# Optimization experiments

Hardware: AMD Instinct MI355X
Metric: run time of the kernel (lower is better)

## Reference

```python
import jax, jax.numpy as jnp
import numpy as np

B, L = 128, 5000
D_MODEL, N_LAYERS, D_STATE, D_INNER, D_CONV, DT_RANK = 8, 4, 16, 16, 3, 1
HID, N_CLASSES = 64, 230


def setup_inputs():
    key = jax.random.key(0)
    ks = iter(jax.random.split(key, 32))
    nrm = lambda shape, s=0.02: jax.random.normal(next(ks), shape, jnp.float32) * s
    return {
        "x": jax.random.uniform(next(ks), (B, L), jnp.float32),
        "idx": jnp.arange(L, dtype=jnp.int32),
        "embed": nrm((L, D_MODEL), 1.0),
        "norm_w": jnp.ones((N_LAYERS, D_MODEL), jnp.float32),
        "in_proj_w": nrm((N_LAYERS, 2 * D_INNER, D_MODEL), 0.2),
        "conv_w": nrm((N_LAYERS, D_INNER, 1, D_CONV), 0.3),
        "conv_b": nrm((N_LAYERS, D_INNER)),
        "x_proj_w": nrm((N_LAYERS, DT_RANK + 2 * D_STATE, D_INNER), 0.2),
        "dt_proj_w": nrm((N_LAYERS, D_INNER, DT_RANK), 0.5),
        "dt_proj_b": nrm((N_LAYERS, D_INNER), 0.1),
        "A_log": jnp.broadcast_to(jnp.log(jnp.arange(1., D_STATE + 1.)), (N_LAYERS, D_INNER, D_STATE)).astype(jnp.float32),
        "Dp": jnp.ones((N_LAYERS, D_INNER), jnp.float32),
        "out_proj_w": nrm((N_LAYERS, D_MODEL, D_INNER), 0.2),
        "c1_w": nrm((HID, D_MODEL, 3), 0.2), "c1_b": nrm((HID,)),
        "c2_w": nrm((HID, HID, 3), 0.1), "c2_b": nrm((HID,)),
        "c3_w": nrm((HID, HID, 3), 0.1), "c3_b": nrm((HID,)),
        "fc_w": nrm((N_CLASSES, HID), 0.1), "fc_b": jnp.zeros((N_CLASSES,), jnp.float32),
    }


def _conv1d(x, w, b, pad, groups=1):
    # x: [B, C, L], w: [O, I/groups, K]
    y = jax.lax.conv_general_dilated(x, w, (1,), [pad], dimension_numbers=("NCH", "OIH", "NCH"), feature_group_count=groups)
    return y + b[None, :, None]


def _rmsnorm(x, w, eps=1e-5):
    return x * jax.lax.rsqrt(jnp.mean(x * x, -1, keepdims=True) + eps) * w


def _selective_scan(u, delta, A, Bm, Cm, Dv):
    # u, delta: [B, L, ED]; A: [ED, N]; Bm, Cm: [B, L, N]
    dA = jnp.exp(delta[..., None] * A)                       # [B, L, ED, N]
    dBu = delta[..., None] * Bm[:, :, None, :] * u[..., None]  # [B, L, ED, N]

    def step(h, t):
        dA_t, dBu_t, c_t = t
        h = dA_t * h + dBu_t                                  # [B, ED, N]
        return h, jnp.einsum("ben,bn->be", h, c_t)

    h0 = jnp.zeros((dA.shape[0], dA.shape[2], dA.shape[3]), u.dtype)
    _, ys = jax.lax.scan(step, h0, (dA.swapaxes(0, 1), dBu.swapaxes(0, 1), Cm.swapaxes(0, 1)))
    return ys.swapaxes(0, 1) + Dv * u


def reference(x, idx, embed, norm_w, in_proj_w, conv_w, conv_b, x_proj_w, dt_proj_w, dt_proj_b, A_log, Dp, out_proj_w, c1_w, c1_b, c2_w, c2_b, c3_w, c3_b, fc_w, fc_b):
    # embedding(idx) broadcast over batch, gated by intensities x
    f = embed[idx][None, :, :] * x[:, :, None]                # [B, L, D_MODEL]
    for l in range(N_LAYERS):
        xn = _rmsnorm(f, norm_w[l])
        xz = xn @ in_proj_w[l].T                              # [B, L, 2*ED]
        xc, z = xz[..., :D_INNER], xz[..., D_INNER:]
        xc = _conv1d(xc.swapaxes(1, 2), conv_w[l], conv_b[l], (D_CONV - 1, 0), D_INNER).swapaxes(1, 2)
        xc = jax.nn.silu(xc)
        dbc = xc @ x_proj_w[l].T                              # [B, L, dt_rank+2N]
        delta = jax.nn.softplus(dbc[..., :DT_RANK] @ dt_proj_w[l].T + dt_proj_b[l])
        Bm = dbc[..., DT_RANK:DT_RANK + D_STATE]
        Cm = dbc[..., DT_RANK + D_STATE:]
        y = _selective_scan(xc, delta, -jnp.exp(A_log[l]), Bm, Cm, Dp[l])
        f = (y * jax.nn.silu(z)) @ out_proj_w[l].T + f        # residual
    feat = f.swapaxes(1, 2)                                   # [B, D_MODEL, L]
    h = jax.nn.relu(_conv1d(feat, c1_w, c1_b, (1, 1)))
    r = jax.nn.relu(_conv1d(h, c2_w, c2_b, (1, 1)))
    r = _conv1d(r, c3_w, c3_b, (1, 1))
    h = jax.nn.relu(h + r)                                    # residual conv block
    pooled = h.mean(-1)                                       # [B, HID]
    return pooled @ fc_w.T + fc_b                             # [B, N_CLASSES]
```

## Files before the change

kernel.cpp:

```cpp
#include <hip/hip_runtime.h>
#include <math.h>

#define B 128
#define L 5000
#define NL 4
#define NCH 50
#define LC 100
#define ST 50
#define HT 128

typedef __attribute__((ext_vector_type(8))) short bf16x8;
typedef __attribute__((ext_vector_type(4))) short short4v;
typedef __attribute__((ext_vector_type(4))) float f32x4;

__device__ __forceinline__ float sigmoidf_(float x){ return 1.f/(1.f+__expf(-x)); }
__device__ __forceinline__ float siluf_(float x){ return x*sigmoidf_(x); }
__device__ __forceinline__ float softplusf_(float x){ return fmaxf(x,0.f) + log1pf(__expf(-fabsf(x))); }
__device__ __forceinline__ short bfc_(float x){
  union { float f; unsigned u; } v; v.f = x;
  unsigned r = v.u + 0x7fffu + ((v.u >> 16) & 1u);
  return (short)(r >> 16);
}
__device__ __forceinline__ float b2f_(short s){
  union { unsigned u; float f; } v; v.u = ((unsigned)(unsigned short)s) << 16;
  return v.f;
}
#define SW(row, col) (((row)<<6) + ((col) ^ (((row)&7)<<3)))

__global__ void k_embed(const float* __restrict__ x, const int* __restrict__ idx,
                        const float* __restrict__ embed, float* __restrict__ f){
  int gid = blockIdx.x*256 + threadIdx.x;
  if (gid >= B*L) return;
  int t = gid % L;
  float xv = x[gid];
  const float* er = embed + (size_t)idx[t]*8;
  float4 e0 = *(const float4*)(er);
  float4 e1 = *(const float4*)(er+4);
  *(float4*)(f + (size_t)gid*8)   = make_float4(e0.x*xv, e0.y*xv, e0.z*xv, e0.w*xv);
  *(float4*)(f + (size_t)gid*8+4) = make_float4(e1.x*xv, e1.y*xv, e1.z*xv, e1.w*xv);
}

__global__ __launch_bounds__(256,4) void k_l1(const float* __restrict__ fin,
    const float* __restrict__ norm_w, const float* __restrict__ in_proj,
    const float* __restrict__ conv_w, const float* __restrict__ conv_b,
    const float* __restrict__ x_proj, const float* __restrict__ dt_w,
    const float* __restrict__ dt_b, const float* __restrict__ A_log,
    float* __restrict__ Sc, float* __restrict__ Pc){
  __shared__ float fsub[52][8], rn[52];
  __shared__ float uL[ST][17];
  __shared__ float2 duL[ST][16];
  __shared__ float BLs[ST][17];
  __shared__ float dbc0[ST];
  int tid = threadIdx.x, ch = blockIdx.x, b = blockIdx.y;
  int e = tid>>4, n = tid&15;
  int ct = tid&15;
  float ipnw_c[8], cwc[3];
  #pragma unroll
  for (int d=0;d<8;d++) ipnw_c[d] = in_proj[ct*8+d]*norm_w[d];
  #pragma unroll
  for (int k=0;k<3;k++) cwc[k] = conv_w[ct*3+k];
  float cbc = conv_b[ct];
  float xp0_c = x_proj[ct];
  float xpB_r[16];
  #pragma unroll
  for (int k=0;k<16;k++) xpB_r[k] = x_proj[(1+ct)*16+k];
  float dtw_e = dt_w[ct], dtb_e = dt_b[ct];
  float a = -__expf(A_log[e*16+n]);
  float h = 0.f, dsum = 0.f;
  int t00 = ch*LC;
  for (int sub=0; sub<LC/ST; sub++){
    int ts = t00 + sub*ST;
    __syncthreads();
    for (int i=tid;i<104;i+=256){ int r=i>>1, half=i&1; int t=ts-2+r;
      *(float4*)&fsub[r][half*4] = (t>=0) ? *(const float4*)&fin[((size_t)b*L+t)*8+half*4]
                                          : make_float4(0.f,0.f,0.f,0.f); }
    __syncthreads();
    if (tid < 52){ float ss=0.f;
      #pragma unroll
      for (int d=0;d<8;d++){ float v=fsub[tid][d]; ss += v*v; }
      rn[tid] = rsqrtf(ss*0.125f + 1e-5f); }
    __syncthreads();
    for (int i=tid;i<ST*16;i+=256){ int j=i>>4;
      float acc = cbc;
      #pragma unroll
      for (int kk=0;kk<3;kk++){
        int r = j + kk;
        float dot=0.f;
        #pragma unroll
        for (int d=0;d<8;d++) dot += ipnw_c[d]*fsub[r][d];
        acc += cwc[kk]*(dot*rn[r]);
      }
      float uv = siluf_(acc);
      uL[j][ct] = uv;
      float pp = xp0_c*uv;
      pp += __shfl_xor(pp, 1, 64);
      pp += __shfl_xor(pp, 2, 64);
      pp += __shfl_xor(pp, 4, 64);
      pp += __shfl_xor(pp, 8, 64);
      if (ct == 0) dbc0[j] = pp;
    }
    __syncthreads();
    for (int i=tid;i<ST*16;i+=256){ int j=i>>4;
      float accB=0.f;
      #pragma unroll
      for (int c=0;c<16;c++) accB += xpB_r[c]*uL[j][c];
      BLs[j][ct] = accB;
      float dd = softplusf_(dbc0[j]*dtw_e + dtb_e);
      duL[j][ct] = make_float2(dd, dd*uL[j][ct]);
    }
    __syncthreads();
    for (int j=0;j<ST;j++){
      float2 du = duL[j][e];
      float bb = BLs[j][n];
      h = __expf(du.x*a)*h + du.y*bb;
      dsum += du.x;
    }
  }
  size_t o = ((size_t)b*NCH + ch)*256 + tid;
  Sc[o] = h;
  Pc[o] = __expf(a*dsum);
}

__global__ __launch_bounds__(256,4) void k_l3(const float* __restrict__ fin, float* __restrict__ fout,
    const float* __restrict__ norm_w, const float* __restrict__ in_proj,
    const float* __restrict__ conv_w, const float* __restrict__ conv_b,
    const float* __restrict__ x_proj, const float* __restrict__ dt_w,
    const float* __restrict__ dt_b, const float* __restrict__ A_log,
    const float* __restrict__ Dp, const float* __restrict__ Sc,
    const float* __restrict__ Pc, const float* __restrict__ ow){
  __shared__ float fsub[52][8], rn[52];
  __shared__ float uL[ST*16], szL[ST*16], yL[ST*16];
  __shared__ float2 duL[ST*16], BCL[ST*16];
  __shared__ float dbc0[ST];
  __shared__ float s_owp[8*17], s_De[16];
  __shared__ float hcL[10*320];
  int tid = threadIdx.x, ch = blockIdx.x, b = blockIdx.y;
  int e = tid>>4, n = tid&15;
  int ct = tid&15;
  int dt8 = tid&7;
  float ipnw_c[8], ipnwz_c[8], cwc[3];
  #pragma unroll
  for (int d=0;d<8;d++){
    ipnw_c[d]  = in_proj[ct*8+d]*norm_w[d];
    ipnwz_c[d] = in_proj[(16+ct)*8+d]*norm_w[d];
  }
  #pragma unroll
  for (int k=0;k<3;k++) cwc[k] = conv_w[ct*3+k];
  float cbc = conv_b[ct];
  float xp0_c = x_proj[ct];
  float xpB_r[16], xpC_r[16];
  #pragma unroll
  for (int k=0;k<16;k++){
    xpB_r[k] = x_proj[(1+ct)*16+k];
    xpC_r[k] = x_proj[(17+ct)*16+k];
  }
  float dtw_e = dt_w[ct], dtb_e = dt_b[ct];
  float a = -__expf(A_log[e*16+n]);
  if (tid < 128) s_owp[(tid>>4)*17 + (tid&15)] = ow[tid];
  if (tid < 16) s_De[tid] = Dp[tid];
  float h = 0.f;
  for (int c2=0; c2<ch; c2++){
    size_t o = ((size_t)b*NCH + c2)*256 + tid;
    h = Pc[o]*h + Sc[o];
  }
  int t00 = ch*LC;
  for (int sub=0; sub<LC/ST; sub++){
    int ts = t00 + sub*ST;
    __syncthreads();
    for (int i=tid;i<104;i+=256){ int r=i>>1, half=i&1; int t=ts-2+r;
      *(float4*)&fsub[r][half*4] = (t>=0) ? *(const float4*)&fin[((size_t)b*L+t)*8+half*4]
                                          : make_float4(0.f,0.f,0.f,0.f); }
    __syncthreads();
    if (tid < 52){ float ss=0.f;
      #pragma unroll
      for (int d=0;d<8;d++){ float v=fsub[tid][d]; ss += v*v; }
      rn[tid] = rsqrtf(ss*0.125f + 1e-5f); }
    __syncthreads();
    for (int i=tid;i<ST*16;i+=256){ int j=i>>4;
      float acc = cbc;
      #pragma unroll
      for (int kk=0;kk<3;kk++){
        int r = j + kk;
        float dot=0.f;
        #pragma unroll
        for (int d=0;d<8;d++) dot += ipnw_c[d]*fsub[r][d];
        acc += cwc[kk]*(dot*rn[r]);
      }
      float uv = siluf_(acc);
      uL[j*16+ct] = uv;
      int r2 = j + 2;
      float dz=0.f;
      #pragma unroll
      for (int d=0;d<8;d++) dz += ipnwz_c[d]*fsub[r2][d];
      szL[j*16+ct] = siluf_(dz*rn[r2]);
      float pp = xp0_c*uv;
      pp += __shfl_xor(pp, 1, 64);
      pp += __shfl_xor(pp, 2, 64);
      pp += __shfl_xor(pp, 4, 64);
      pp += __shfl_xor(pp, 8, 64);
      if (ct == 0) dbc0[j] = pp;
    }
    __syncthreads();
    for (int i=tid;i<ST*16;i+=256){ int j=i>>4;
      f32x4 u0 = *(const f32x4*)&uL[j*16];
      f32x4 u1 = *(const f32x4*)&uL[j*16+4];
      f32x4 u2 = *(const f32x4*)&uL[j*16+8];
      f32x4 u3 = *(const f32x4*)&uL[j*16+12];
      float accB=0.f, accC=0.f;
      #pragma unroll
      for (int c=0;c<4;c++){
        accB += xpB_r[c]*u0[c] + xpB_r[4+c]*u1[c] + xpB_r[8+c]*u2[c] + xpB_r[12+c]*u3[c];
        accC += xpC_r[c]*u0[c] + xpC_r[4+c]*u1[c] + xpC_r[8+c]*u2[c] + xpC_r[12+c]*u3[c];
      }
      BCL[j*16+ct] = make_float2(accB, accC);
      float dd = softplusf_(dbc0[j]*dtw_e + dtb_e);
      duL[j*16+ct] = make_float2(dd, dd*uL[j*16+ct]);
    }
    __syncthreads();
    for (int q=0; q<ST/10; q++){
      #pragma unroll
      for (int j2=0; j2<10; j2++){
        int j = q*10 + j2;
        float2 du = duL[j*16+e];
        float2 bc = BCL[j*16+n];
        h = __expf(du.x*a)*h + du.y*bc.x;
        hcL[j2*320 + e*20 + n] = h*bc.y;
      }
      __syncthreads();
      if (tid < 160){
        int jj = tid>>4, ee = tid&15;
        int j = q*10 + jj;
        const f32x4* hp = (const f32x4*)&hcL[jj*320 + ee*20];
        f32x4 p0 = hp[0], p1 = hp[1], p2 = hp[2], p3 = hp[3];
        float s = ((p0[0]+p0[1])+(p0[2]+p0[3])) + ((p1[0]+p1[1])+(p1[2]+p1[3]))
                + ((p2[0]+p2[1])+(p2[2]+p2[3])) + ((p3[0]+p3[1])+(p3[2]+p3[3]));
        yL[j*16+ee] = (s + s_De[ee]*uL[j*16+ee]) * szL[j*16+ee];
      }
      __syncthreads();
    }
    for (int i=tid;i<ST*8;i+=256){ int j=i>>3;
      size_t fi = ((size_t)b*L + ts + j)*8 + dt8;
      float acc = fsub[j+2][dt8];
      f32x4 y0 = *(const f32x4*)&yL[j*16];
      f32x4 y1 = *(const f32x4*)&yL[j*16+4];
      f32x4 y2 = *(const f32x4*)&yL[j*16+8];
      f32x4 y3 = *(const f32x4*)&yL[j*16+12];
      #pragma unroll
      for (int c=0;c<4;c++)
        acc += s_owp[dt8*17+c]*y0[c] + s_owp[dt8*17+4+c]*y1[c]
             + s_owp[dt8*17+8+c]*y2[c] + s_owp[dt8*17+12+c]*y3[c];
      fout[fi] = acc;
    }
  }
}

__global__ void k_wt(const float* __restrict__ c1w, const float* __restrict__ c2w,
                     const float* __restrict__ c3w, short* __restrict__ wt1b,
                     short* __restrict__ wt2b, short* __restrict__ wt3b){
  int idx = blockIdx.x*256 + threadIdx.x;
  if (idx < 2048){
    int c = idx >> 5, m = idx & 31;
    int kk = m >> 3, d = m & 7;
    wt1b[idx] = (kk < 3) ? bfc_(c1w[c*24 + d*3 + kk]) : (short)0;
  } else if (idx < 2048 + 12288){
    int i = idx - 2048;
    int c = i / 192, rem = i % 192;
    int k = rem >> 6, ci = rem & 63;
    wt2b[i] = bfc_(c2w[c*192 + ci*3 + k]);
  } else if (idx < 2048 + 24576){
    int i = idx - 2048 - 12288;
    int c = i / 192, rem = i % 192;
    int k = rem >> 6, ci = rem & 63;
    wt3b[i] = bfc_(c3w[c*192 + ci*3 + k]);
  }
}

__global__ __launch_bounds__(256) void k_head(const float* __restrict__ f,
   const short* __restrict__ wt1b, const float* __restrict__ c1b,
   const short* __restrict__ wt2b, const float* __restrict__ c2b,
   const short* __restrict__ wt3b, const float* __restrict__ c3b,
   float* __restrict__ pooled){
  __shared__ short fs_b[146*8];
  __shared__ short h1t[146*64];
  __shared__ short h2t[130*64];
  int tid  = threadIdx.x;
  int b    = blockIdx.y;
  int t0   = blockIdx.x * HT;
  int lane = tid & 63;
  int w    = tid >> 6;
  int cb   = w*16;
  int lc   = lane & 15, g = lane >> 4;

  for (int task = tid; task < 146*8; task += 256){
    int r = task >> 3, d = task & 7;
    int t = t0 - 3 + r;
    float v = (r < 134 && t >= 0 && t < L) ? f[((size_t)b*L + t)*8 + d] : 0.f;
    fs_b[task] = bfc_(v);
  }
  for (int i = tid; i < 14*64; i += 256){
    int row = 132 + (i>>6), col = i&63;
    h1t[SW(row, col)] = 0;
  }
  __syncthreads();

  {
    bf16x8 a1 = *(const bf16x8*)(wt1b + (cb + lc)*32 + g*8);
    f32x4 bias1 = *(const f32x4*)(c1b + cb + (g<<2));
    #pragma unroll
    for (int nt=0; nt<9; nt++){
      int tcol = nt*16 + lc;
      bf16x8 bv = {0,0,0,0,0,0,0,0};
      if (g < 3) bv = *(bf16x8*)&fs_b[(tcol+g)*8];
      f32x4 acc = {0.f,0.f,0.f,0.f};
      acc = __builtin_amdgcn_mfma_f32_16x16x32_bf16(a1, bv, acc, 0, 0, 0);
      if (tcol < 132){
        int t1 = t0 - 2 + tcol;
        bool v = (t1 >= 0 && t1 < L);
        short4v pk;
        #pragma unroll
        for (int reg=0;reg<4;reg++)
          pk[reg] = bfc_(v ? fmaxf(acc[reg] + bias1[reg], 0.f) : 0.f);
        *(short4v*)&h1t[SW(tcol, cb + (g<<2))] = pk;
      }
    }
  }
  __syncthreads();

  {
    const short* wA = wt2b + (cb + lc)*192 + g*8;
    bf16x8 a2[6];
    #pragma unroll
    for (int s=0;s<6;s++) a2[s] = *(const bf16x8*)(wA + 32*s);
    f32x4 bias2 = *(const f32x4*)(c2b + cb + (g<<2));
    #pragma unroll
    for (int nt=0; nt<9; nt++){
      f32x4 acc = {0.f,0.f,0.f,0.f};
      #pragma unroll
      for (int s=0;s<6;s++){
        int k = s>>1, ci0 = (s&1)*32;
        int jr = nt*16 + lc + k;
        bf16x8 bfr = *(bf16x8*)&h1t[SW(jr, ci0 + g*8)];
        acc = __builtin_amdgcn_mfma_f32_16x16x32_bf16(a2[s], bfr, acc, 0, 0, 0);
      }
      int tr = nt*16 + lc;
      if (tr < 130){
        int tg = t0 - 1 + tr;
        bool v = (tg >= 0 && tg < L);
        short4v pk;
        #pragma unroll
        for (int reg=0;reg<4;reg++)
          pk[reg] = bfc_(v ? fmaxf(acc[reg] + bias2[reg], 0.f) : 0.f);
        *(short4v*)&h2t[SW(tr, cb + (g<<2))] = pk;
      }
    }
  }
  __syncthreads();

  {
    const short* wA = wt3b + (cb + lc)*192 + g*8;
    bf16x8 a3[6];
    #pragma unroll
    for (int s=0;s<6;s++) a3[s] = *(const bf16x8*)(wA + 32*s);
    f32x4 bias3 = *(const f32x4*)(c3b + cb + (g<<2));
    int c0 = cb + (g<<2);
    float pool[4] = {0.f,0.f,0.f,0.f};
    #pragma unroll
    for (int nt=0; nt<8; nt++){
      f32x4 acc = {0.f,0.f,0.f,0.f};
      #pragma unroll
      for (int s=0;s<6;s++){
        int k = s>>1, ci0 = (s&1)*32;
        int jr = nt*16 + lc + k;
        bf16x8 bfr = *(bf16x8*)&h2t[SW(jr, ci0 + g*8)];
        acc = __builtin_amdgcn_mfma_f32_16x16x32_bf16(a3[s], bfr, acc, 0, 0, 0);
      }
      int t = t0 + nt*16 + lc;
      short4v hres = *(short4v*)&h1t[SW(nt*16 + lc + 2, c0)];
      if (t < L){
        #pragma unroll
        for (int reg=0;reg<4;reg++)
          pool[reg] += fmaxf(b2f_(hres[reg]) + acc[reg] + bias3[reg], 0.f);
      }
    }
    #pragma unroll
    for (int m=1; m<16; m<<=1){
      #pragma unroll
      for (int reg=0;reg<4;reg++) pool[reg] += __shfl_xor(pool[reg], m, 64);
    }
    if (lc == 0){
      #pragma unroll
      for (int reg=0;reg<4;reg++) atomicAdd(&pooled[b*64 + c0 + reg], pool[reg]);
    }
  }
}

__global__ void k_fc(const float* __restrict__ pooled, const float* __restrict__ fcw,
                     const float* __restrict__ fcb, float* __restrict__ out){
  int gid = blockIdx.x*256 + threadIdx.x;
  if (gid >= B*230) return;
  int b = gid / 230, j = gid % 230;
  const float* p = pooled + b*64;
  const float* wv = fcw + j*64;
  float a = 0.f;
  #pragma unroll
  for (int c=0;c<64;c++) a += p[c]*wv[c];
  out[gid] = a*(1.f/(float)L) + fcb[j];
}

extern "C" void kernel_launch(void* const* d_in, const int* in_sizes, int n_in,
                              void* d_out, int out_size, void* d_ws, size_t ws_size,
                              hipStream_t stream){
  const float* x      = (const float*)d_in[0];
  const int*   idx    = (const int*)  d_in[1];
  const float* embed  = (const float*)d_in[2];
  const float* norm_w = (const float*)d_in[3];
  const float* in_proj= (const float*)d_in[4];
  const float* conv_w = (const float*)d_in[5];
  const float* conv_b = (const float*)d_in[6];
  const float* x_proj = (const float*)d_in[7];
  const float* dt_w   = (const float*)d_in[8];
  const float* dt_b   = (const float*)d_in[9];
  const float* A_log  = (const float*)d_in[10];
  const float* Dp     = (const float*)d_in[11];
  const float* out_w  = (const float*)d_in[12];
  const float* c1w    = (const float*)d_in[13];
  const float* c1b    = (const float*)d_in[14];
  const float* c2w    = (const float*)d_in[15];
  const float* c2b    = (const float*)d_in[16];
  const float* c3w    = (const float*)d_in[17];
  const float* c3b    = (const float*)d_in[18];
  const float* fcw    = (const float*)d_in[19];
  const float* fcb    = (const float*)d_in[20];
  float* out = (float*)d_out;

  float* ws = (float*)d_ws;
  float* f0     = ws;
  float* f1     = f0 + 5120000;
  float* Sc     = f1 + 5120000;
  float* Pc     = Sc + 1638400;
  float* pooled = Pc + 1638400;
  short* wt1b   = (short*)(pooled + 8192);
  short* wt2b   = wt1b + 2048;
  short* wt3b   = wt2b + 12288;

  k_wt<<<104,256,0,stream>>>(c1w, c2w, c3w, wt1b, wt2b, wt3b);
  k_embed<<<2500,256,0,stream>>>(x, idx, embed, f0);
  for (int l=0;l<NL;l++){
    const float* fin = (l & 1) ? f1 : f0;
    float*       fo  = (l & 1) ? f0 : f1;
    k_l1<<<dim3(NCH,B),256,0,stream>>>(fin, norm_w + l*8, in_proj + l*256, conv_w + l*48,
         conv_b + l*16, x_proj + l*528, dt_w + l*16, dt_b + l*16, A_log + l*256, Sc, Pc);
    k_l3<<<dim3(NCH,B),256,0,stream>>>(fin, fo, norm_w + l*8, in_proj + l*256, conv_w + l*48,
         conv_b + l*16, x_proj + l*528, dt_w + l*16, dt_b + l*16, A_log + l*256,
         Dp + l*16, Sc, Pc, out_w + l*128);
  }
  (void)hipMemsetAsync(pooled, 0, B*64*sizeof(float), stream);
  k_head<<<dim3((L+HT-1)/HT,B),256,0,stream>>>(f0, wt1b, c1b, wt2b, c2b, wt3b, c3b, pooled);
  k_fc<<<(B*230+255)/256,256,0,stream>>>(pooled, fcw, fcb, out);
}
```

Baseline: 1.217 ms.

## Materialize per-step scan inputs in k_l1 and reload them in k_l3

```diff
diff --git a/kernel.cpp b/kernel.cpp
--- a/kernel.cpp
+++ b/kernel.cpp
@@ -45,7 +45,8 @@
     const float* __restrict__ conv_w, const float* __restrict__ conv_b,
     const float* __restrict__ x_proj, const float* __restrict__ dt_w,
     const float* __restrict__ dt_b, const float* __restrict__ A_log,
-    float* __restrict__ Sc, float* __restrict__ Pc){
+    float* __restrict__ Sc, float* __restrict__ Pc,
+    float2* __restrict__ duA, float2* __restrict__ BCA, float* __restrict__ szA){
   __shared__ float fsub[52][8], rn[52];
   __shared__ float uL[ST][17];
   __shared__ float2 duL[ST][16];
@@ -54,90 +55,6 @@
   int tid = threadIdx.x, ch = blockIdx.x, b = blockIdx.y;
   int e = tid>>4, n = tid&15;
   int ct = tid&15;
-  float ipnw_c[8], cwc[3];
-  #pragma unroll
-  for (int d=0;d<8;d++) ipnw_c[d] = in_proj[ct*8+d]*norm_w[d];
-  #pragma unroll
-  for (int k=0;k<3;k++) cwc[k] = conv_w[ct*3+k];
-  float cbc = conv_b[ct];
-  float xp0_c = x_proj[ct];
-  float xpB_r[16];
-  #pragma unroll
-  for (int k=0;k<16;k++) xpB_r[k] = x_proj[(1+ct)*16+k];
-  float dtw_e = dt_w[ct], dtb_e = dt_b[ct];
-  float a = -__expf(A_log[e*16+n]);
-  float h = 0.f, dsum = 0.f;
-  int t00 = ch*LC;
-  for (int sub=0; sub<LC/ST; sub++){
-    int ts = t00 + sub*ST;
-    __syncthreads();
-    for (int i=tid;i<104;i+=256){ int r=i>>1, half=i&1; int t=ts-2+r;
-      *(float4*)&fsub[r][half*4] = (t>=0) ? *(const float4*)&fin[((size_t)b*L+t)*8+half*4]
-                                          : make_float4(0.f,0.f,0.f,0.f); }
-    __syncthreads();
-    if (tid < 52){ float ss=0.f;
-      #pragma unroll
-      for (int d=0;d<8;d++){ float v=fsub[tid][d]; ss += v*v; }
-      rn[tid] = rsqrtf(ss*0.125f + 1e-5f); }
-    __syncthreads();
-    for (int i=tid;i<ST*16;i+=256){ int j=i>>4;
-      float acc = cbc;
-      #pragma unroll
-      for (int kk=0;kk<3;kk++){
-        int r = j + kk;
-        float dot=0.f;
-        #pragma unroll
-        for (int d=0;d<8;d++) dot += ipnw_c[d]*fsub[r][d];
-        acc += cwc[kk]*(dot*rn[r]);
-      }
-      float uv = siluf_(acc);
-      uL[j][ct] = uv;
-      float pp = xp0_c*uv;
-      pp += __shfl_xor(pp, 1, 64);
-      pp += __shfl_xor(pp, 2, 64);
-      pp += __shfl_xor(pp, 4, 64);
-      pp += __shfl_xor(pp, 8, 64);
-      if (ct == 0) dbc0[j] = pp;
-    }
-    __syncthreads();
-    for (int i=tid;i<ST*16;i+=256){ int j=i>>4;
-      float accB=0.f;
-      #pragma unroll
-      for (int c=0;c<16;c++) accB += xpB_r[c]*uL[j][c];
-      BLs[j][ct] = accB;
-      float dd = softplusf_(dbc0[j]*dtw_e + dtb_e);
-      duL[j][ct] = make_float2(dd, dd*uL[j][ct]);
-    }
-    __syncthreads();
-    for (int j=0;j<ST;j++){
-      float2 du = duL[j][e];
-      float bb = BLs[j][n];
-      h = __expf(du.x*a)*h + du.y*bb;
-      dsum += du.x;
-    }
-  }
-  size_t o = ((size_t)b*NCH + ch)*256 + tid;
-  Sc[o] = h;
-  Pc[o] = __expf(a*dsum);
-}
-
-__global__ __launch_bounds__(256,4) void k_l3(const float* __restrict__ fin, float* __restrict__ fout,
-    const float* __restrict__ norm_w, const float* __restrict__ in_proj,
-    const float* __restrict__ conv_w, const float* __restrict__ conv_b,
-    const float* __restrict__ x_proj, const float* __restrict__ dt_w,
-    const float* __restrict__ dt_b, const float* __restrict__ A_log,
-    const float* __restrict__ Dp, const float* __restrict__ Sc,
-    const float* __restrict__ Pc, const float* __restrict__ ow){
-  __shared__ float fsub[52][8], rn[52];
-  __shared__ float uL[ST*16], szL[ST*16], yL[ST*16];
-  __shared__ float2 duL[ST*16], BCL[ST*16];
-  __shared__ float dbc0[ST];
-  __shared__ float s_owp[8*17], s_De[16];
-  __shared__ float hcL[10*320];
-  int tid = threadIdx.x, ch = blockIdx.x, b = blockIdx.y;
-  int e = tid>>4, n = tid&15;
-  int ct = tid&15;
-  int dt8 = tid&7;
   float ipnw_c[8], ipnwz_c[8], cwc[3];
   #pragma unroll
   for (int d=0;d<8;d++){
@@ -156,6 +73,88 @@
   }
   float dtw_e = dt_w[ct], dtb_e = dt_b[ct];
   float a = -__expf(A_log[e*16+n]);
+  float h = 0.f, dsum = 0.f;
+  int t00 = ch*LC;
+  for (int sub=0; sub<LC/ST; sub++){
+    int ts = t00 + sub*ST;
+    __syncthreads();
+    for (int i=tid;i<104;i+=256){ int r=i>>1, half=i&1; int t=ts-2+r;
+      *(float4*)&fsub[r][half*4] = (t>=0) ? *(const float4*)&fin[((size_t)b*L+t)*8+half*4]
+                                          : make_float4(0.f,0.f,0.f,0.f); }
+    __syncthreads();
+    if (tid < 52){ float ss=0.f;
+      #pragma unroll
+      for (int d=0;d<8;d++){ float v=fsub[tid][d]; ss += v*v; }
+      rn[tid] = rsqrtf(ss*0.125f + 1e-5f); }
+    __syncthreads();
+    for (int i=tid;i<ST*16;i+=256){ int j=i>>4;
+      float acc = cbc;
+      #pragma unroll
+      for (int kk=0;kk<3;kk++){
+        int r = j + kk;
+        float dot=0.f;
+        #pragma unroll
+        for (int d=0;d<8;d++) dot += ipnw_c[d]*fsub[r][d];
+        acc += cwc[kk]*(dot*rn[r]);
+      }
+      float uv = siluf_(acc);
+      uL[j][ct] = uv;
+      int r2 = j + 2;
+      float dz=0.f;
+      #pragma unroll
+      for (int d=0;d<8;d++) dz += ipnwz_c[d]*fsub[r2][d];
+      szA[((size_t)b*L + ts + j)*16 + ct] = siluf_(dz*rn[r2]);
+      float pp = xp0_c*uv;
+      pp += __shfl_xor(pp, 1, 64);
+      pp += __shfl_xor(pp, 2, 64);
+      pp += __shfl_xor(pp, 4, 64);
+      pp += __shfl_xor(pp, 8, 64);
+      if (ct == 0) dbc0[j] = pp;
+    }
+    __syncthreads();
+    for (int i=tid;i<ST*16;i+=256){ int j=i>>4;
+      float accB=0.f, accC=0.f;
+      #pragma unroll
+      for (int c=0;c<16;c++){
+        float uv2 = uL[j][c];
+        accB += xpB_r[c]*uv2;
+        accC += xpC_r[c]*uv2;
+      }
+      BLs[j][ct] = accB;
+      float dd = softplusf_(dbc0[j]*dtw_e + dtb_e);
+      float uv = uL[j][ct];
+      duL[j][ct] = make_float2(dd, dd*uv);
+      size_t gi = ((size_t)b*L + ts + j)*16 + ct;
+      BCA[gi] = make_float2(accB, accC);
+      duA[gi] = make_float2(dd, uv);
+    }
+    __syncthreads();
+    for (int j=0;j<ST;j++){
+      float2 du = duL[j][e];
+      float bb = BLs[j][n];
+      h = __expf(du.x*a)*h + du.y*bb;
+      dsum += du.x;
+    }
+  }
+  size_t o = ((size_t)b*NCH + ch)*256 + tid;
+  Sc[o] = h;
+  Pc[o] = __expf(a*dsum);
+}
+
+__global__ __launch_bounds__(256,4) void k_l3(const float* __restrict__ fin, float* __restrict__ fout,
+    const float* __restrict__ A_log, const float* __restrict__ Dp,
+    const float* __restrict__ Sc, const float* __restrict__ Pc,
+    const float* __restrict__ ow,
+    const float2* __restrict__ duA, const float2* __restrict__ BCA,
+    const float* __restrict__ szA){
+  __shared__ float2 duL[ST*16], BCL[ST*16];
+  __shared__ float uLs[ST*16], szL[ST*16], yL[ST*16];
+  __shared__ float hcL[10*320];
+  __shared__ float s_owp[8*17], s_De[16];
+  int tid = threadIdx.x, ch = blockIdx.x, b = blockIdx.y;
+  int e = tid>>4, n = tid&15;
+  int dt8 = tid&7;
+  float a = -__expf(A_log[e*16+n]);
   if (tid < 128) s_owp[(tid>>4)*17 + (tid&15)] = ow[tid];
   if (tid < 16) s_De[tid] = Dp[tid];
   float h = 0.f;
@@ -167,54 +166,22 @@
   for (int sub=0; sub<LC/ST; sub++){
     int ts = t00 + sub*ST;
     __syncthreads();
-    for (int i=tid;i<104;i+=256){ int r=i>>1, half=i&1; int t=ts-2+r;
-      *(float4*)&fsub[r][half*4] = (t>=0) ? *(const float4*)&fin[((size_t)b*L+t)*8+half*4]
-                                          : make_float4(0.f,0.f,0.f,0.f); }
-    __syncthreads();
-    if (tid < 52){ float ss=0.f;
-      #pragma unroll
-      for (int d=0;d<8;d++){ float v=fsub[tid][d]; ss += v*v; }
-      rn[tid] = rsqrtf(ss*0.125f + 1e-5f); }
-    __syncthreads();
-    for (int i=tid;i<ST*16;i+=256){ int j=i>>4;
-      float acc = cbc;
-      #pragma unroll
-      for (int kk=0;kk<3;kk++){
-        int r = j + kk;
-        float dot=0.f;
-        #pragma unroll
-        for (int d=0;d<8;d++) dot += ipnw_c[d]*fsub[r][d];
-        acc += cwc[kk]*(dot*rn[r]);
-      }
-      float uv = siluf_(acc);
-      uL[j*16+ct] = uv;
-      int r2 = j + 2;
-      float dz=0.f;
-      #pragma unroll
-      for (int d=0;d<8;d++) dz += ipnwz_c[d]*fsub[r2][d];
-      szL[j*16+ct] = siluf_(dz*rn[r2]);
-      float pp = xp0_c*uv;
-      pp += __shfl_xor(pp, 1, 64);
-      pp += __shfl_xor(pp, 2, 64);
-      pp += __shfl_xor(pp, 4, 64);
-      pp += __shfl_xor(pp, 8, 64);
-      if (ct == 0) dbc0[j] = pp;
-    }
-    __syncthreads();
-    for (int i=tid;i<ST*16;i+=256){ int j=i>>4;
-      f32x4 u0 = *(const f32x4*)&uL[j*16];
-      f32x4 u1 = *(const f32x4*)&uL[j*16+4];
-      f32x4 u2 = *(const f32x4*)&uL[j*16+8];
-      f32x4 u3 = *(const f32x4*)&uL[j*16+12];
-      float accB=0.f, accC=0.f;
-      #pragma unroll
-      for (int c=0;c<4;c++){
-        accB += xpB_r[c]*u0[c] + xpB_r[4+c]*u1[c] + xpB_r[8+c]*u2[c] + xpB_r[12+c]*u3[c];
-        accC += xpC_r[c]*u0[c] + xpC_r[4+c]*u1[c] + xpC_r[8+c]*u2[c] + xpC_r[12+c]*u3[c];
-      }
-      BCL[j*16+ct] = make_float2(accB, accC);
-      float dd = softplusf_(dbc0[j]*dtw_e + dtb_e);
-      duL[j*16+ct] = make_float2(dd, dd*uL[j*16+ct]);
+    const f32x4* duG = (const f32x4*)(duA + ((size_t)b*L + ts)*16);
+    const f32x4* bcG = (const f32x4*)(BCA + ((size_t)b*L + ts)*16);
+    for (int i=tid;i<400;i+=256){
+      f32x4 v = duG[i];
+      int bidx = i*2;
+      duL[bidx]   = make_float2(v[0], v[0]*v[1]);
+      duL[bidx+1] = make_float2(v[2], v[2]*v[3]);
+      uLs[bidx]   = v[1];
+      uLs[bidx+1] = v[3];
+      f32x4 wv = bcG[i];
+      BCL[bidx]   = make_float2(wv[0], wv[1]);
+      BCL[bidx+1] = make_float2(wv[2], wv[3]);
+    }
+    const f32x4* szG = (const f32x4*)(szA + ((size_t)b*L + ts)*16);
+    for (int i=tid;i<200;i+=256){
+      *(f32x4*)&szL[i*4] = szG[i];
     }
     __syncthreads();
     for (int q=0; q<ST/10; q++){
@@ -234,13 +201,13 @@
         f32x4 p0 = hp[0], p1 = hp[1], p2 = hp[2], p3 = hp[3];
         float s = ((p0[0]+p0[1])+(p0[2]+p0[3])) + ((p1[0]+p1[1])+(p1[2]+p1[3]))
                 + ((p2[0]+p2[1])+(p2[2]+p2[3])) + ((p3[0]+p3[1])+(p3[2]+p3[3]));
-        yL[j*16+ee] = (s + s_De[ee]*uL[j*16+ee]) * szL[j*16+ee];
+        yL[j*16+ee] = (s + s_De[ee]*uLs[j*16+ee]) * szL[j*16+ee];
       }
       __syncthreads();
     }
     for (int i=tid;i<ST*8;i+=256){ int j=i>>3;
       size_t fi = ((size_t)b*L + ts + j)*8 + dt8;
-      float acc = fsub[j+2][dt8];
+      float acc = fin[fi];
       f32x4 y0 = *(const f32x4*)&yL[j*16];
       f32x4 y1 = *(const f32x4*)&yL[j*16+4];
       f32x4 y2 = *(const f32x4*)&yL[j*16+8];
@@ -439,7 +406,10 @@
   float* Sc     = f1 + 5120000;
   float* Pc     = Sc + 1638400;
   float* pooled = Pc + 1638400;
-  short* wt1b   = (short*)(pooled + 8192);
+  float2* duA   = (float2*)(pooled + 8192);
+  float2* BCA   = duA + 10240000;
+  float* szA    = (float*)(BCA + 10240000);
+  short* wt1b   = (short*)(szA + 10240000);
   short* wt2b   = wt1b + 2048;
   short* wt3b   = wt2b + 12288;
 
@@ -449,10 +419,10 @@
     const float* fin = (l & 1) ? f1 : f0;
     float*       fo  = (l & 1) ? f0 : f1;
     k_l1<<<dim3(NCH,B),256,0,stream>>>(fin, norm_w + l*8, in_proj + l*256, conv_w + l*48,
-         conv_b + l*16, x_proj + l*528, dt_w + l*16, dt_b + l*16, A_log + l*256, Sc, Pc);
-    k_l3<<<dim3(NCH,B),256,0,stream>>>(fin, fo, norm_w + l*8, in_proj + l*256, conv_w + l*48,
          conv_b + l*16, x_proj + l*528, dt_w + l*16, dt_b + l*16, A_log + l*256,
-         Dp + l*16, Sc, Pc, out_w + l*128);
+         Sc, Pc, duA, BCA, szA);
+    k_l3<<<dim3(NCH,B),256,0,stream>>>(fin, fo, A_log + l*256, Dp + l*16, Sc, Pc,
+         out_w + l*128, duA, BCA, szA);
   }
   (void)hipMemsetAsync(pooled, 0, B*64*sizeof(float), stream);
   k_head<<<dim3((L+HT-1)/HT,B),256,0,stream>>>(f0, wt1b, c1b, wt2b, c2b, wt3b, c3b, pooled);
```

New measurement: 1.146 ms. 1.06x faster.
